# Kernel optimization log

Hardware: AMD Instinct MI355X
Metric: run time of the kernel (lower is better)

## Reference

```python
import jax, jax.numpy as jnp
import numpy as np

IN_FEATURES = 4096
OUT_FEATURES = 11008
GROUP_SIZE = 128
N_HIGH = 1024   # int(0.25*4096)//8*8
N_LOW = 3072    # (4096-1024)//8*8
M_TOKENS = 64


def unpack_6bit(packed, original_k):
    # packed: [K*3//4, N] uint8 values stored as int32
    _, N = packed.shape
    p = packed.reshape(original_k // 4, 3, N)
    b0, b1, b2 = p[:, 0], p[:, 1], p[:, 2]
    v0 = b0 & 63
    v1 = ((b0 >> 6) & 3) | ((b1 & 15) << 2)
    v2 = ((b1 >> 4) & 15) | ((b2 & 3) << 4)
    v3 = (b2 >> 2) & 63
    return jnp.stack([v0, v1, v2, v3], axis=1).reshape(original_k, N)


def unpack_5bit(packed, original_k):
    # packed: [K*5//8, N]
    _, N = packed.shape
    p = packed.reshape(original_k // 8, 5, N)
    b = [p[:, i] for i in range(5)]
    v0 = b[0] & 31
    v1 = ((b[0] >> 5) & 7) | ((b[1] & 3) << 3)
    v2 = (b[1] >> 2) & 31
    v3 = ((b[1] >> 7) & 1) | ((b[2] & 15) << 1)
    v4 = ((b[2] >> 4) & 15) | ((b[3] & 1) << 4)
    v5 = (b[3] >> 1) & 31
    v6 = ((b[3] >> 6) & 3) | ((b[4] & 7) << 2)
    v7 = (b[4] >> 3) & 31
    return jnp.stack([v0, v1, v2, v3, v4, v5, v6, v7], axis=1).reshape(original_k, N)


def dequant_region(W_q, scales, half_range):
    # W_q: [K, N] ints in [0, 2*half_range]; scales: [num_groups, N]
    K, N = W_q.shape
    G = scales.shape[0]
    Wg = (W_q.astype(jnp.float32) - float(half_range)).reshape(G, GROUP_SIZE, N)
    return (Wg * scales[:, None, :]).reshape(K, N)


def setup_inputs() -> dict:
    key = jax.random.key(0)
    ks = jax.random.split(key, 7)
    x = jax.random.normal(ks[0], (M_TOKENS, IN_FEATURES), dtype=jnp.float32)
    W_high_packed = jax.random.randint(ks[1], (N_HIGH * 3 // 4, OUT_FEATURES), 0, 256, dtype=jnp.int32)
    W_low_packed = jax.random.randint(ks[2], (N_LOW * 5 // 8, OUT_FEATURES), 0, 256, dtype=jnp.int32)
    scales_high = jax.random.uniform(ks[3], (N_HIGH // GROUP_SIZE, OUT_FEATURES), dtype=jnp.float32) * 0.02 + 1e-4
    scales_low = jax.random.uniform(ks[4], (N_LOW // GROUP_SIZE, OUT_FEATURES), dtype=jnp.float32) * 0.02 + 1e-4
    col_indices = jax.random.permutation(ks[5], IN_FEATURES).astype(jnp.int32)
    bias = jax.random.normal(ks[6], (OUT_FEATURES,), dtype=jnp.float32) * 0.02
    return {"x": x, "W_high_packed": W_high_packed, "W_low_packed": W_low_packed,
            "scales_high": scales_high, "scales_low": scales_low,
            "col_indices": col_indices, "bias": bias}


def reference(x, W_high_packed, W_low_packed, scales_high, scales_low, col_indices, bias):
    # Unpack mixed 6-bit / 5-bit weights and group-dequantize.
    Wq_high = unpack_6bit(W_high_packed, N_HIGH)          # [1024, N], 0..63
    Wq_low = unpack_5bit(W_low_packed, N_LOW)             # [3072, N], 0..31
    W_high = dequant_region(Wq_high, scales_high, 31)     # 6-bit half_range = 31
    W_low = dequant_region(Wq_low, scales_low, 15)        # 5-bit half_range = 15
    # Column-sensitivity reorder of activations, then split high/low regions.
    x_perm = x[:, col_indices]                            # [M, K]
    x_high = x_perm[:, :N_HIGH]
    x_low = x_perm[:, N_HIGH:N_HIGH + N_LOW]
    out = x_high @ W_high + x_low @ W_low + bias          # [M, N]
    return out
```

## Files before the change

kernel.cpp:

```cpp
#include <hip/hip_runtime.h>


#define NFEAT 11008
#define KTOT  4096

typedef _Float16 half8 __attribute__((ext_vector_type(8)));
typedef _Float16 half2 __attribute__((ext_vector_type(2)));
typedef float    f32x4 __attribute__((ext_vector_type(4)));
typedef int      i32x4 __attribute__((ext_vector_type(4)));

union H8 { half8 v; half2 h[4]; _Float16 e[8]; };

__device__ __forceinline__ half2 dq2(int a, int b, half2 off, half2 s) {
    unsigned u = 0x64006400u | (unsigned)a | ((unsigned)b << 16);
    half2 h = __builtin_bit_cast(half2, u);
    return (h - off) * s;
}

__global__ __launch_bounds__(256) void prep_xfrag(const float* __restrict__ x,
                                                  const int* __restrict__ col,
                                                  _Float16* __restrict__ xfrag) {
    int u  = blockIdx.x * 256 + threadIdx.x;
    int l  = u & 63;
    int mt = (u >> 6) & 3;
    int s  = u >> 8;
    int m  = mt * 16 + (l & 15);
    int kb = s * 32 + ((l >> 4) << 3);
    H8 w;
#pragma unroll
    for (int j = 0; j < 8; ++j)
        w.e[j] = (_Float16)x[m * KTOT + col[kb + j]];
    *(half8*)(xfrag + (size_t)u * 8) = w.v;
}

template <bool HIGH>
__global__ __launch_bounds__(256, 4) void gemm_kernel(const int* __restrict__ W,
                                                      const float* __restrict__ S,
                                                      const _Float16* __restrict__ xfrag,
                                                      float* __restrict__ dst,
                                                      int titers, int sg_off,
                                                      int atomic_mode) {
    const int n0   = blockIdx.x * 64;
    const int tid  = threadIdx.x;
    const int lane = tid & 63;
    const int wave = tid >> 6;
    const int cg   = tid & 15;
    const int kg   = tid >> 4;
    const int kgl  = kg & 3;
    const int colb = n0 + cg * 4;
    const int kbase = blockIdx.y * titers * 128;

    __shared__ _Float16 lds[2 * 8192];
    const int wchunk0 = ((cg >> 2) * 4 + (kg >> 2)) * 64 + kgl * 16 + (cg & 3) * 4;
    const int laneX   = lane ^ (lane >> 4);

    f32x4 acc[4];
#pragma unroll
    for (int i = 0; i < 4; ++i) acc[i] = (f32x4){0.f, 0.f, 0.f, 0.f};

    i32x4 R[6];
    f32x4 s4;

    auto load_tile = [&](int t) {
        const int kb = kbase + t * 128;
        if constexpr (HIGH) {
            const int* p = W + (size_t)((kb >> 2) * 3 + kg * 6) * NFEAT + colb;
#pragma unroll
            for (int r = 0; r < 6; ++r) R[r] = *(const i32x4*)(p + (size_t)r * NFEAT);
        } else {
            const int* p = W + (size_t)((kb >> 3) * 5 + kg * 5) * NFEAT + colb;
#pragma unroll
            for (int r = 0; r < 5; ++r) R[r] = *(const i32x4*)(p + (size_t)r * NFEAT);
        }
        s4 = *(const f32x4*)(S + (size_t)(kb >> 7) * NFEAT + colb);
    };

    auto dq_store = [&](int buf) {
        _Float16* base = lds + (buf << 13);
        const _Float16 offv = HIGH ? (_Float16)1055.0f : (_Float16)1039.0f;
        const half2 off = {offv, offv};
#pragma unroll
        for (int cc = 0; cc < 4; ++cc) {
            int v0, v1, v2, v3, v4, v5, v6, v7;
            if constexpr (HIGH) {
                int b0 = R[0][cc], b1 = R[1][cc], b2 = R[2][cc],
                    b3 = R[3][cc], b4 = R[4][cc], b5 = R[5][cc];
                v0 = b0 & 63;
                v1 = ((b0 >> 6) & 3) | ((b1 & 15) << 2);
                v2 = ((b1 >> 4) & 15) | ((b2 & 3) << 4);
                v3 = (b2 >> 2) & 63;
                v4 = b3 & 63;
                v5 = ((b3 >> 6) & 3) | ((b4 & 15) << 2);
                v6 = ((b4 >> 4) & 15) | ((b5 & 3) << 4);
                v7 = (b5 >> 2) & 63;
            } else {
                int b0 = R[0][cc], b1 = R[1][cc], b2 = R[2][cc],
                    b3 = R[3][cc], b4 = R[4][cc];
                v0 = b0 & 31;
                v1 = ((b0 >> 5) & 7) | ((b1 & 3) << 3);
                v2 = (b1 >> 2) & 31;
                v3 = ((b1 >> 7) & 1) | ((b2 & 15) << 1);
                v4 = ((b2 >> 4) & 15) | ((b3 & 1) << 4);
                v5 = (b3 >> 1) & 31;
                v6 = ((b3 >> 6) & 3) | ((b4 & 7) << 2);
                v7 = (b4 >> 3) & 31;
            }
            _Float16 sc = (_Float16)s4[cc];
            half2 s2 = {sc, sc};
            H8 w;
            w.h[0] = dq2(v0, v1, off, s2);
            w.h[1] = dq2(v2, v3, off, s2);
            w.h[2] = dq2(v4, v5, off, s2);
            w.h[3] = dq2(v6, v7, off, s2);
            *(half8*)(base + (size_t)(wchunk0 + (cc ^ kgl)) * 8) = w.v;
        }
    };

    auto do_mfma = [&](int buf, int t) {
        const _Float16* Bb = lds + (buf << 13);
        const int sg = sg_off + (kbase >> 5) + t * 4;
        half8 a[4];
#pragma unroll
        for (int q = 0; q < 4; ++q)
            a[q] = *(const half8*)(xfrag + (size_t)(((sg + q) * 4 + wave) * 64 + lane) * 8);
#pragma unroll
        for (int q = 0; q < 4; ++q) {
#pragma unroll
            for (int nt = 0; nt < 4; ++nt) {
                half8 b = *(const half8*)(Bb + (size_t)((nt * 4 + q) * 64 + laneX) * 8);
                acc[nt] = __builtin_amdgcn_mfma_f32_16x16x32_f16(a[q], b, acc[nt], 0, 0, 0);
            }
        }
    };

    load_tile(0);
    int buf = 0;
    for (int t = 0; t < titers; ++t) {
        dq_store(buf);
        __syncthreads();
        if (t + 1 < titers) load_tile(t + 1);
        do_mfma(buf, t);
        buf ^= 1;
    }

    const int rb = wave * 16 + ((lane >> 4) << 2);
    const int cb = lane & 15;
    if (atomic_mode) {
#pragma unroll
        for (int j = 0; j < 4; ++j)
#pragma unroll
            for (int r = 0; r < 4; ++r)
                atomicAdd(&dst[(size_t)(rb + r) * NFEAT + n0 + j * 16 + cb], acc[j][r]);
    } else {
        float* o = dst + (size_t)blockIdx.y * 64 * NFEAT;
#pragma unroll
        for (int j = 0; j < 4; ++j)
#pragma unroll
            for (int r = 0; r < 4; ++r)
                o[(size_t)(rb + r) * NFEAT + n0 + j * 16 + cb] = acc[j][r];
    }
}

__global__ __launch_bounds__(256) void reduce_out(const float* __restrict__ part,
                                                  const float* __restrict__ bias,
                                                  float* __restrict__ out, int P) {
    const int idx = blockIdx.x * 256 + threadIdx.x;
    const int f   = idx * 4;
    const int n   = f % NFEAT;
    f32x4 s = *(const f32x4*)(bias + n);
    for (int p = 0; p < P; ++p)
        s += *(const f32x4*)(part + (size_t)p * 704512 + f);
    *(f32x4*)(out + f) = s;
}

__global__ __launch_bounds__(256) void init_bias(const float* __restrict__ bias,
                                                 float* __restrict__ out) {
    const int idx = blockIdx.x * 256 + threadIdx.x;
    out[idx] = bias[idx % NFEAT];
}

extern "C" void kernel_launch(void* const* d_in, const int* in_sizes, int n_in,
                              void* d_out, int out_size, void* d_ws, size_t ws_size,
                              hipStream_t stream) {
    const float* x    = (const float*)d_in[0];
    const int*   Wh   = (const int*)d_in[1];
    const int*   Wl   = (const int*)d_in[2];
    const float* sh   = (const float*)d_in[3];
    const float* sl   = (const float*)d_in[4];
    const int*   col  = (const int*)d_in[5];
    const float* bias = (const float*)d_in[6];
    float* out = (float*)d_out;

    _Float16* xfrag = (_Float16*)d_ws;
    const size_t xb      = (size_t)64 * KTOT * sizeof(_Float16);
    const size_t pstride = (size_t)64 * NFEAT;

    prep_xfrag<<<128, 256, 0, stream>>>(x, col, xfrag);

    if (ws_size >= xb + 8 * pstride * sizeof(float)) {
        float* part = (float*)((char*)d_ws + xb);
        gemm_kernel<true><<<dim3(172, 2), 256, 0, stream>>>(Wh, sh, xfrag, part, 4, 0, 0);
        gemm_kernel<false><<<dim3(172, 6), 256, 0, stream>>>(Wl, sl, xfrag,
                                                             part + 2 * pstride, 4, 32, 0);
        reduce_out<<<688, 256, 0, stream>>>(part, bias, out, 8);
    } else if (ws_size >= xb + 4 * pstride * sizeof(float)) {
        float* part = (float*)((char*)d_ws + xb);
        gemm_kernel<true><<<dim3(172, 1), 256, 0, stream>>>(Wh, sh, xfrag, part, 8, 0, 0);
        gemm_kernel<false><<<dim3(172, 3), 256, 0, stream>>>(Wl, sl, xfrag,
                                                             part + pstride, 8, 32, 0);
        reduce_out<<<688, 256, 0, stream>>>(part, bias, out, 4);
    } else {
        init_bias<<<2752, 256, 0, stream>>>(bias, out);
        gemm_kernel<true><<<dim3(172, 2), 256, 0, stream>>>(Wh, sh, xfrag, out, 4, 0, 1);
        gemm_kernel<false><<<dim3(172, 6), 256, 0, stream>>>(Wl, sl, xfrag, out, 4, 32, 1);
    }
}
```

Baseline: 185.5 us.

## Dequantize weights directly into MFMA B registers, dropping LDS staging; merge high/low GEMMs

The GEMM no longer stages dequantized weights in shared memory. Each lane now loads its own packed weight bytes, dequantizes them straight into an MFMA B operand, and keeps a two-stage register prefetch of weights, scales and activation fragments, so the __syncthreads and LDS round trip go away. The separate 6-bit and 5-bit kernels are merged into one launch that picks the region per K-chunk. The cost is narrower scalar global loads (one int per row per lane instead of int4 vectors) and per-wave loads of the activation fragments, which may reduce coalescing and raise register pressure.

```diff
diff --git a/kernel.cpp b/kernel.cpp
--- a/kernel.cpp
+++ b/kernel.cpp
@@ -7,7 +7,6 @@
 typedef _Float16 half8 __attribute__((ext_vector_type(8)));
 typedef _Float16 half2 __attribute__((ext_vector_type(2)));
 typedef float    f32x4 __attribute__((ext_vector_type(4)));
-typedef int      i32x4 __attribute__((ext_vector_type(4)));
 
 union H8 { half8 v; half2 h[4]; _Float16 e[8]; };
 
@@ -34,130 +33,116 @@
 }
 
 template <bool HIGH>
-__global__ __launch_bounds__(256, 4) void gemm_kernel(const int* __restrict__ W,
-                                                      const float* __restrict__ S,
+__device__ __forceinline__ void run_chunk(const int* __restrict__ W,
+                                          const float* __restrict__ S,
+                                          const _Float16* __restrict__ xfrag,
+                                          int kloc, int sgbase,
+                                          int n, int quad, int lane,
+                                          f32x4 acc[4]) {
+    constexpr int NR = HIGH ? 6 : 5;
+    int   raw[2][6];
+    float sc[2];
+    half8 a[2][4];
+
+    auto issue = [&](int t, int st) {
+        const int k0  = kloc + t * 32 + quad * 8;
+        const int row = HIGH ? 3 * (k0 >> 2) : 5 * (k0 >> 3);
+        const int* p  = W + (size_t)row * NFEAT + n;
+#pragma unroll
+        for (int r = 0; r < NR; ++r) raw[st][r] = p[(size_t)r * NFEAT];
+        sc[st] = S[(size_t)((kloc + t * 32) >> 7) * NFEAT + n];
+        const int sg = sgbase + t;
+#pragma unroll
+        for (int mt = 0; mt < 4; ++mt)
+            a[st][mt] = *(const half8*)(xfrag + (size_t)((sg * 4 + mt) * 64 + lane) * 8);
+    };
+
+    auto consume = [&](int st) {
+        int v0, v1, v2, v3, v4, v5, v6, v7;
+        if constexpr (HIGH) {
+            int b0 = raw[st][0], b1 = raw[st][1], b2 = raw[st][2],
+                b3 = raw[st][3], b4 = raw[st][4], b5 = raw[st][5];
+            v0 = b0 & 63;
+            v1 = ((b0 >> 6) & 3) | ((b1 & 15) << 2);
+            v2 = ((b1 >> 4) & 15) | ((b2 & 3) << 4);
+            v3 = (b2 >> 2) & 63;
+            v4 = b3 & 63;
+            v5 = ((b3 >> 6) & 3) | ((b4 & 15) << 2);
+            v6 = ((b4 >> 4) & 15) | ((b5 & 3) << 4);
+            v7 = (b5 >> 2) & 63;
+        } else {
+            int b0 = raw[st][0], b1 = raw[st][1], b2 = raw[st][2],
+                b3 = raw[st][3], b4 = raw[st][4];
+            v0 = b0 & 31;
+            v1 = ((b0 >> 5) & 7) | ((b1 & 3) << 3);
+            v2 = (b1 >> 2) & 31;
+            v3 = ((b1 >> 7) & 1) | ((b2 & 15) << 1);
+            v4 = ((b2 >> 4) & 15) | ((b3 & 1) << 4);
+            v5 = (b3 >> 1) & 31;
+            v6 = ((b3 >> 6) & 3) | ((b4 & 7) << 2);
+            v7 = (b4 >> 3) & 31;
+        }
+        const _Float16 ofv = HIGH ? (_Float16)1055.0f : (_Float16)1039.0f;
+        const half2 off = {ofv, ofv};
+        _Float16 s1 = (_Float16)sc[st];
+        half2 s2 = {s1, s1};
+        H8 w;
+        w.h[0] = dq2(v0, v1, off, s2);
+        w.h[1] = dq2(v2, v3, off, s2);
+        w.h[2] = dq2(v4, v5, off, s2);
+        w.h[3] = dq2(v6, v7, off, s2);
+#pragma unroll
+        for (int mt = 0; mt < 4; ++mt)
+            acc[mt] = __builtin_amdgcn_mfma_f32_16x16x32_f16(a[st][mt], w.v, acc[mt], 0, 0, 0);
+    };
+
+    issue(0, 0);
+#pragma unroll
+    for (int t = 0; t < 16; ++t) {
+        if (t + 1 < 16) issue(t + 1, (t + 1) & 1);
+        consume(t & 1);
+    }
+}
+
+__global__ __launch_bounds__(256, 4) void gemm_kernel(const int* __restrict__ Wh,
+                                                      const int* __restrict__ Wl,
+                                                      const float* __restrict__ sh,
+                                                      const float* __restrict__ sl,
                                                       const _Float16* __restrict__ xfrag,
                                                       float* __restrict__ dst,
-                                                      int titers, int sg_off,
-                                                      int atomic_mode) {
-    const int n0   = blockIdx.x * 64;
-    const int tid  = threadIdx.x;
-    const int lane = tid & 63;
-    const int wave = tid >> 6;
-    const int cg   = tid & 15;
-    const int kg   = tid >> 4;
-    const int kgl  = kg & 3;
-    const int colb = n0 + cg * 4;
-    const int kbase = blockIdx.y * titers * 128;
-
-    __shared__ _Float16 lds[2 * 8192];
-    const int wchunk0 = ((cg >> 2) * 4 + (kg >> 2)) * 64 + kgl * 16 + (cg & 3) * 4;
-    const int laneX   = lane ^ (lane >> 4);
+                                                      int nsub, int atomic_mode) {
+    const int lane = threadIdx.x & 63;
+    const int wave = threadIdx.x >> 6;
+    const int quad = lane >> 4;
+    const int n    = blockIdx.x * 64 + wave * 16 + (lane & 15);
 
     f32x4 acc[4];
 #pragma unroll
     for (int i = 0; i < 4; ++i) acc[i] = (f32x4){0.f, 0.f, 0.f, 0.f};
 
-    i32x4 R[6];
-    f32x4 s4;
-
-    auto load_tile = [&](int t) {
-        const int kb = kbase + t * 128;
-        if constexpr (HIGH) {
-            const int* p = W + (size_t)((kb >> 2) * 3 + kg * 6) * NFEAT + colb;
-#pragma unroll
-            for (int r = 0; r < 6; ++r) R[r] = *(const i32x4*)(p + (size_t)r * NFEAT);
-        } else {
-            const int* p = W + (size_t)((kb >> 3) * 5 + kg * 5) * NFEAT + colb;
-#pragma unroll
-            for (int r = 0; r < 5; ++r) R[r] = *(const i32x4*)(p + (size_t)r * NFEAT);
-        }
-        s4 = *(const f32x4*)(S + (size_t)(kb >> 7) * NFEAT + colb);
-    };
-
-    auto dq_store = [&](int buf) {
-        _Float16* base = lds + (buf << 13);
-        const _Float16 offv = HIGH ? (_Float16)1055.0f : (_Float16)1039.0f;
-        const half2 off = {offv, offv};
-#pragma unroll
-        for (int cc = 0; cc < 4; ++cc) {
-            int v0, v1, v2, v3, v4, v5, v6, v7;
-            if constexpr (HIGH) {
-                int b0 = R[0][cc], b1 = R[1][cc], b2 = R[2][cc],
-                    b3 = R[3][cc], b4 = R[4][cc], b5 = R[5][cc];
-                v0 = b0 & 63;
-                v1 = ((b0 >> 6) & 3) | ((b1 & 15) << 2);
-                v2 = ((b1 >> 4) & 15) | ((b2 & 3) << 4);
-                v3 = (b2 >> 2) & 63;
-                v4 = b3 & 63;
-                v5 = ((b3 >> 6) & 3) | ((b4 & 15) << 2);
-                v6 = ((b4 >> 4) & 15) | ((b5 & 3) << 4);
-                v7 = (b5 >> 2) & 63;
-            } else {
-                int b0 = R[0][cc], b1 = R[1][cc], b2 = R[2][cc],
-                    b3 = R[3][cc], b4 = R[4][cc];
-                v0 = b0 & 31;
-                v1 = ((b0 >> 5) & 7) | ((b1 & 3) << 3);
-                v2 = (b1 >> 2) & 31;
-                v3 = ((b1 >> 7) & 1) | ((b2 & 15) << 1);
-                v4 = ((b2 >> 4) & 15) | ((b3 & 1) << 4);
-                v5 = (b3 >> 1) & 31;
-                v6 = ((b3 >> 6) & 3) | ((b4 & 7) << 2);
-                v7 = (b4 >> 3) & 31;
-            }
-            _Float16 sc = (_Float16)s4[cc];
-            half2 s2 = {sc, sc};
-            H8 w;
-            w.h[0] = dq2(v0, v1, off, s2);
-            w.h[1] = dq2(v2, v3, off, s2);
-            w.h[2] = dq2(v4, v5, off, s2);
-            w.h[3] = dq2(v6, v7, off, s2);
-            *(half8*)(base + (size_t)(wchunk0 + (cc ^ kgl)) * 8) = w.v;
-        }
-    };
-
-    auto do_mfma = [&](int buf, int t) {
-        const _Float16* Bb = lds + (buf << 13);
-        const int sg = sg_off + (kbase >> 5) + t * 4;
-        half8 a[4];
-#pragma unroll
-        for (int q = 0; q < 4; ++q)
-            a[q] = *(const half8*)(xfrag + (size_t)(((sg + q) * 4 + wave) * 64 + lane) * 8);
-#pragma unroll
-        for (int q = 0; q < 4; ++q) {
-#pragma unroll
-            for (int nt = 0; nt < 4; ++nt) {
-                half8 b = *(const half8*)(Bb + (size_t)((nt * 4 + q) * 64 + laneX) * 8);
-                acc[nt] = __builtin_amdgcn_mfma_f32_16x16x32_f16(a[q], b, acc[nt], 0, 0, 0);
-            }
-        }
-    };
-
-    load_tile(0);
-    int buf = 0;
-    for (int t = 0; t < titers; ++t) {
-        dq_store(buf);
-        __syncthreads();
-        if (t + 1 < titers) load_tile(t + 1);
-        do_mfma(buf, t);
-        buf ^= 1;
+    for (int s = 0; s < nsub; ++s) {
+        const int kglob  = (blockIdx.y * nsub + s) * 512;
+        const int sgbase = kglob >> 5;
+        if (kglob < 1024)
+            run_chunk<true >(Wh, sh, xfrag, kglob,        sgbase, n, quad, lane, acc);
+        else
+            run_chunk<false>(Wl, sl, xfrag, kglob - 1024, sgbase, n, quad, lane, acc);
     }
 
-    const int rb = wave * 16 + ((lane >> 4) << 2);
-    const int cb = lane & 15;
+    const int rb = quad << 2;
     if (atomic_mode) {
 #pragma unroll
-        for (int j = 0; j < 4; ++j)
+        for (int mt = 0; mt < 4; ++mt)
 #pragma unroll
             for (int r = 0; r < 4; ++r)
-                atomicAdd(&dst[(size_t)(rb + r) * NFEAT + n0 + j * 16 + cb], acc[j][r]);
+                atomicAdd(&dst[(size_t)(mt * 16 + rb + r) * NFEAT + n], acc[mt][r]);
     } else {
         float* o = dst + (size_t)blockIdx.y * 64 * NFEAT;
 #pragma unroll
-        for (int j = 0; j < 4; ++j)
+        for (int mt = 0; mt < 4; ++mt)
 #pragma unroll
             for (int r = 0; r < 4; ++r)
-                o[(size_t)(rb + r) * NFEAT + n0 + j * 16 + cb] = acc[j][r];
+                o[(size_t)(mt * 16 + rb + r) * NFEAT + n] = acc[mt][r];
     }
 }
 
@@ -166,8 +151,8 @@
                                                   float* __restrict__ out, int P) {
     const int idx = blockIdx.x * 256 + threadIdx.x;
     const int f   = idx * 4;
-    const int n   = f % NFEAT;
-    f32x4 s = *(const f32x4*)(bias + n);
+    const int nn  = f % NFEAT;
+    f32x4 s = *(const f32x4*)(bias + nn);
     for (int p = 0; p < P; ++p)
         s += *(const f32x4*)(part + (size_t)p * 704512 + f);
     *(f32x4*)(out + f) = s;
@@ -199,19 +184,14 @@
 
     if (ws_size >= xb + 8 * pstride * sizeof(float)) {
         float* part = (float*)((char*)d_ws + xb);
-        gemm_kernel<true><<<dim3(172, 2), 256, 0, stream>>>(Wh, sh, xfrag, part, 4, 0, 0);
-        gemm_kernel<false><<<dim3(172, 6), 256, 0, stream>>>(Wl, sl, xfrag,
-                                                             part + 2 * pstride, 4, 32, 0);
+        gemm_kernel<<<dim3(172, 8), 256, 0, stream>>>(Wh, Wl, sh, sl, xfrag, part, 1, 0);
         reduce_out<<<688, 256, 0, stream>>>(part, bias, out, 8);
     } else if (ws_size >= xb + 4 * pstride * sizeof(float)) {
         float* part = (float*)((char*)d_ws + xb);
-        gemm_kernel<true><<<dim3(172, 1), 256, 0, stream>>>(Wh, sh, xfrag, part, 8, 0, 0);
-        gemm_kernel<false><<<dim3(172, 3), 256, 0, stream>>>(Wl, sl, xfrag,
-                                                             part + pstride, 8, 32, 0);
+        gemm_kernel<<<dim3(172, 4), 256, 0, stream>>>(Wh, Wl, sh, sl, xfrag, part, 2, 0);
         reduce_out<<<688, 256, 0, stream>>>(part, bias, out, 4);
     } else {
         init_bias<<<2752, 256, 0, stream>>>(bias, out);
-        gemm_kernel<true><<<dim3(172, 2), 256, 0, stream>>>(Wh, sh, xfrag, out, 4, 0, 1);
-        gemm_kernel<false><<<dim3(172, 6), 256, 0, stream>>>(Wl, sl, xfrag, out, 4, 32, 1);
+        gemm_kernel<<<dim3(172, 8), 256, 0, stream>>>(Wh, Wl, sh, sl, xfrag, out, 1, 1);
     }
 }
```

Measured after the change: 195.7 us. 1.06x slower.
